# Kernel tuning notes

Measured on AMD Instinct MI355X. Metric: run time of the kernel, lower is better.

## Reference

```python
import jax, jax.numpy as jnp
import numpy as np

DIM = 2048
BATCH = 16384
EPS = 1e-12


def setup_inputs() -> dict:
    key = jax.random.key(0)
    ks = jax.random.split(key, 12)
    d = DIM
    inp = {
        "h_final": jax.random.normal(ks[0], (BATCH, d), dtype=jnp.float32),
        "v_claim": jax.random.normal(ks[1], (BATCH, d), dtype=jnp.float32),
        "v_doc": jax.random.normal(ks[2], (BATCH, d), dtype=jnp.float32),
        # feature_extractor: Linear(d+3, d) -> ReLU -> Linear(d, d//2) -> ReLU
        "W1": jax.random.normal(ks[3], (d + 3, d), dtype=jnp.float32) / np.sqrt(d + 3),
        "b1": jnp.zeros((d,), dtype=jnp.float32),
        "W2": jax.random.normal(ks[4], (d, d // 2), dtype=jnp.float32) / np.sqrt(d),
        "b2": jnp.zeros((d // 2,), dtype=jnp.float32),
        # retrieval head: Linear(d//2, 1) -> Sigmoid
        "Wr": jax.random.normal(ks[5], (d // 2, 1), dtype=jnp.float32) / np.sqrt(d // 2),
        "br": jnp.zeros((1,), dtype=jnp.float32),
    }
    return inp


def reference(h_final, v_claim, v_doc, W1, b1, W2, b2, Wr, br):
    # L2-normalize claim/doc vectors (F.normalize with eps clamp)
    cn = v_claim / jnp.maximum(jnp.linalg.norm(v_claim, axis=-1, keepdims=True), EPS)
    dn = v_doc / jnp.maximum(jnp.linalg.norm(v_doc, axis=-1, keepdims=True), EPS)
    # alignment = cosine similarity (vectors already unit norm) -> [B, 1]
    align = jnp.sum(cn * dn, axis=-1, keepdims=True)
    # divergence = 1 - alignment; tension = divergence^2
    div = 1.0 - align
    tens = div * div
    features = jnp.concatenate([h_final, align, div, tens], axis=-1)  # [B, d+3]
    h = jax.nn.relu(features @ W1 + b1)
    shared = jax.nn.relu(h @ W2 + b2)  # [B, d//2]
    out = jax.nn.sigmoid(shared @ Wr + br)  # [B, 1] (task='retrieval')
    return out
```

## Files before the change

### kernel.cpp

```cpp
#include <hip/hip_runtime.h>
#include <hip/hip_bf16.h>
#include <stdint.h>

#define BATCH 16384
#define DIM   2048
#define DIM2  1024

typedef __attribute__((ext_vector_type(8))) short short8;
typedef __attribute__((ext_vector_type(4))) float f32x4;

__device__ __forceinline__ ushort f2bf(float f) {
  uint32_t u = __float_as_uint(f);
  u += 0x7fffu + ((u >> 16) & 1u);
  return (ushort)(u >> 16);
}
__device__ __forceinline__ float bf2f(ushort h) {
  return __uint_as_float(((uint32_t)h) << 16);
}

__device__ __forceinline__ void gload_lds16(const void* g, void* l) {
  __builtin_amdgcn_global_load_lds(
      (__attribute__((address_space(1))) void*)g,
      (__attribute__((address_space(3))) void*)l,
      16, 0, 0);
}

__device__ __forceinline__ f32x4 MFMA(short8 a, short8 b, f32x4 c) {
  return __builtin_amdgcn_mfma_f32_16x16x32_bf16(a, b, c, 0, 0, 0);
}

__global__ void __launch_bounds__(256) cos_kernel(const float* __restrict__ vc,
                                                  const float* __restrict__ vd,
                                                  float* __restrict__ feats) {
  const int w = threadIdx.x >> 6, l = threadIdx.x & 63;
  const int row = blockIdx.x * 4 + w;
  const float4* c = (const float4*)(vc + (size_t)row * DIM);
  const float4* d = (const float4*)(vd + (size_t)row * DIM);
  float4 ca[8], da[8];
#pragma unroll
  for (int j = 0; j < 8; ++j) ca[j] = c[j * 64 + l];
#pragma unroll
  for (int j = 0; j < 8; ++j) da[j] = d[j * 64 + l];
  float dot = 0.f, c2 = 0.f, d2 = 0.f;
#pragma unroll
  for (int j = 0; j < 8; ++j) {
    float4 a = ca[j], b = da[j];
    dot += a.x * b.x + a.y * b.y + a.z * b.z + a.w * b.w;
    c2  += a.x * a.x + a.y * a.y + a.z * a.z + a.w * a.w;
    d2  += b.x * b.x + b.y * b.y + b.z * b.z + b.w * b.w;
  }
#pragma unroll
  for (int off = 32; off >= 1; off >>= 1) {
    dot += __shfl_xor(dot, off, 64);
    c2  += __shfl_xor(c2, off, 64);
    d2  += __shfl_xor(d2, off, 64);
  }
  if (l == 0) {
    float nc = fmaxf(sqrtf(c2), 1e-12f);
    float nd = fmaxf(sqrtf(d2), 1e-12f);
    float align = dot / (nc * nd);
    float dv = 1.f - align;
    feats[row] = align;
    feats[BATCH + row] = dv;
    feats[2 * BATCH + row] = dv * dv;
  }
}

__global__ void __launch_bounds__(256) cvt_kernel(const float* __restrict__ in,
                                                  ushort* __restrict__ out) {
  const int i0 = blockIdx.x * 256 + threadIdx.x;
  const int S = 8192 * 256;
  const float4* p = (const float4*)in;
  uint2* o = (uint2*)out;
  float4 f[4];
#pragma unroll
  for (int j = 0; j < 4; ++j) f[j] = p[i0 + j * S];
#pragma unroll
  for (int j = 0; j < 4; ++j) {
    uint2 u;
    u.x = (uint32_t)f2bf(f[j].x) | ((uint32_t)f2bf(f[j].y) << 16);
    u.y = (uint32_t)f2bf(f[j].z) | ((uint32_t)f2bf(f[j].w) << 16);
    o[i0 + j * S] = u;
  }
}

__global__ void __launch_bounds__(256) transW(const float* __restrict__ W,
                                              ushort* __restrict__ WT,
                                              int K, int N) {
  __shared__ float tile[32][33];
  int t = threadIdx.x;
  int tx = t & 31, ty = t >> 5;
  int c0 = blockIdx.x * 32, r0 = blockIdx.y * 32;
#pragma unroll
  for (int p = 0; p < 4; ++p)
    tile[ty + p * 8][tx] = W[(size_t)(r0 + ty + p * 8) * N + c0 + tx];
  __syncthreads();
#pragma unroll
  for (int p = 0; p < 4; ++p) {
    int rr = ty + p * 8;
    WT[(size_t)(c0 + rr) * K + r0 + tx] = f2bf(tile[tx][rr]);
  }
}

template <int MODE, int N>
__global__ void __launch_bounds__(512, 1) gemm256(const ushort* __restrict__ A,
                                                  const ushort* __restrict__ BT,
                                                  ushort* __restrict__ C,
                                                  const float* __restrict__ feats,
                                                  const float* __restrict__ wex,
                                                  const float* __restrict__ bias) {
  constexpr int K = 2048;
  constexpr int NT = K / 64;
  __shared__ __align__(16) char lds[131072];
  const int tid = threadIdx.x;
  const int l = tid & 63, w = tid >> 6;
  const int wr = w >> 2, wc = w & 3;
  const int l4 = l & 15, lhi = l >> 4;

  constexpr int GX = N / 256;
  const int bid = blockIdx.x;
  const int xcd = bid & 7;
  const int s = bid >> 3;
  const int tx = s % GX;
  const int ty = xcd * 8 + s / GX;
  const size_t rowBase = (size_t)ty * 256;
  const int colBase = tx * 256;

  const int swz = (l4 & 7) << 4;
  const int aoffBase = l4 * 128 + ((wr * 64 + lhi * 16) ^ swz);
  const int boffBase = ((wc & 1) * 64 + l4) * 128 + (((wc >> 1) * 64 + lhi * 16) ^ swz);

  const char* pAs[2];
  const char* pBs[2];
#pragma unroll
  for (int c = 0; c < 2; ++c) {
    int o = c * 8192 + tid * 16;
    int r = o >> 7, b0 = o & 127;
    int bsw = b0 ^ ((r & 7) << 4);
    int hb = bsw >> 6, cb = bsw & 63;
    pAs[c] = (const char*)A + (rowBase + hb * 128 + r) * (2 * K) + cb;
    pBs[c] = (const char*)BT + ((size_t)colBase + hb * 128 + r) * (2 * K) + cb;
  }
  const int ldso0 = w * 1024;
  const int ldso1 = 8192 + w * 1024;

#define STAGE(srcT, destPar, M, kh)                                          \
  do {                                                                       \
    char* dst_ = lds + (destPar) * 65536 + (kh) * 32768 + (M) * 16384;       \
    const char* s0_ = ((M) ? pBs[0] : pAs[0]) + (srcT) * 128 + (kh) * 64;    \
    const char* s1_ = ((M) ? pBs[1] : pAs[1]) + (srcT) * 128 + (kh) * 64;    \
    gload_lds16(s0_, dst_ + ldso0);                                          \
    gload_lds16(s1_, dst_ + ldso1);                                          \
    asm volatile("" ::: "memory");                                           \
  } while (0)

#define LOADA(q, d, kh)                                                      \
  do {                                                                       \
    const char* sb_ = lds + (d) * 65536 + (kh) * 32768;                      \
    aq[0] = *(const short8*)(sb_ + ((q) * 4 + 0) * 2048 + aoffBase);         \
    aq[1] = *(const short8*)(sb_ + ((q) * 4 + 1) * 2048 + aoffBase);         \
    aq[2] = *(const short8*)(sb_ + ((q) * 4 + 2) * 2048 + aoffBase);         \
    aq[3] = *(const short8*)(sb_ + ((q) * 4 + 3) * 2048 + aoffBase);         \
  } while (0)

#define LOADB(d, kh)                                                         \
  do {                                                                       \
    const char* sb_ = lds + (d) * 65536 + (kh) * 32768 + 16384;              \
    bq[0] = *(const short8*)(sb_ + 0 * 2048 + boffBase);                     \
    bq[1] = *(const short8*)(sb_ + 1 * 2048 + boffBase);                     \
    bq[2] = *(const short8*)(sb_ + 2 * 2048 + boffBase);                     \
    bq[3] = *(const short8*)(sb_ + 3 * 2048 + boffBase);                     \
  } while (0)

#define MF(q)                                                                \
  do {                                                                       \
    _Pragma("unroll") for (int j_ = 0; j_ < 4; ++j_)                         \
        _Pragma("unroll") for (int n_ = 0; n_ < 4; ++n_)                     \
            acc[(q) * 4 + j_][n_] = MFMA(aq[j_], bq[n_], acc[(q) * 4 + j_][n_]); \
  } while (0)

#define BAR()     __builtin_amdgcn_s_barrier()
#define MEMF()    asm volatile("" ::: "memory")
#define VM8()     asm volatile("s_waitcnt vmcnt(8)" ::: "memory")
#define PRIO(x)   __builtin_amdgcn_s_setprio(x)

  f32x4 acc[8][4];
#pragma unroll
  for (int i = 0; i < 8; ++i)
#pragma unroll
    for (int j = 0; j < 4; ++j) acc[i][j] = (f32x4){0.f, 0.f, 0.f, 0.f};

  STAGE(0, 0, 0, 0);
  STAGE(0, 0, 1, 0);
  STAGE(0, 0, 0, 1);
  STAGE(0, 0, 1, 1);
  STAGE(1, 1, 0, 0);
  STAGE(1, 1, 1, 0);
  VM8();
  BAR();
  MEMF();

  for (int I = 0; I < NT / 2; ++I) {
    const int o = 2 * I + 1;
    const int e2 = (2 * I + 2 < NT) ? 2 * I + 2 : 0;
    const int o2 = (2 * I + 3 < NT) ? 2 * I + 3 : 0;
    short8 aq[4], bq[4];
    LOADB(0, 0);
    LOADA(0, 0, 0);
    STAGE(o, 1, 0, 1);
    PRIO(1); MF(0); PRIO(0);
    MEMF(); BAR(); MEMF();
    LOADA(1, 0, 0);
    STAGE(o, 1, 1, 1);
    PRIO(1); MF(1); PRIO(0);
    VM8();
    MEMF(); BAR(); MEMF();
    LOADB(0, 1);
    LOADA(0, 0, 1);
    STAGE(e2, 0, 0, 0);
    PRIO(1); MF(0); PRIO(0);
    MEMF(); BAR(); MEMF();
    LOADA(1, 0, 1);
    STAGE(e2, 0, 1, 0);
    PRIO(1); MF(1); PRIO(0);
    VM8();
    MEMF(); BAR(); MEMF();
    LOADB(1, 0);
    LOADA(0, 1, 0);
    STAGE(e2, 0, 0, 1);
    PRIO(1); MF(0); PRIO(0);
    MEMF(); BAR(); MEMF();
    LOADA(1, 1, 0);
    STAGE(e2, 0, 1, 1);
    PRIO(1); MF(1); PRIO(0);
    VM8();
    MEMF(); BAR(); MEMF();
    LOADB(1, 1);
    LOADA(0, 1, 1);
    STAGE(o2, 1, 0, 0);
    PRIO(1); MF(0); PRIO(0);
    MEMF(); BAR(); MEMF();
    LOADA(1, 1, 1);
    STAGE(o2, 1, 1, 0);
    PRIO(1); MF(1); PRIO(0);
    VM8();
    MEMF(); BAR(); MEMF();
  }
  asm volatile("s_waitcnt vmcnt(0)" ::: "memory");

  int ccv[4];
  float bb[4], wa[4], wb2[4], wc3[4];
#pragma unroll
  for (int n = 0; n < 4; ++n) {
    int cc = colBase + wc * 64 + n * 16 + l4;
    ccv[n] = cc;
    bb[n] = bias[cc];
    if (MODE == 1) {
      wa[n] = wex[cc]; wb2[n] = wex[2048 + cc]; wc3[n] = wex[4096 + cc];
    } else {
      wa[n] = 0.f; wb2[n] = 0.f; wc3[n] = 0.f;
    }
  }
  const int lhi4 = lhi * 4;
#pragma unroll
  for (int m = 0; m < 8; ++m) {
#pragma unroll
    for (int r = 0; r < 4; ++r) {
      size_t rr = rowBase + wr * 128 + m * 16 + lhi4 + r;
      float f1 = 0.f, f2 = 0.f, f3 = 0.f;
      if (MODE == 1) {
        f1 = feats[rr]; f2 = feats[BATCH + rr]; f3 = feats[2 * BATCH + rr];
      }
#pragma unroll
      for (int n = 0; n < 4; ++n) {
        float v = acc[m][n][r] + bb[n];
        if (MODE == 1) v += f1 * wa[n] + f2 * wb2[n] + f3 * wc3[n];
        v = fmaxf(v, 0.f);
        C[rr * N + ccv[n]] = f2bf(v);
      }
    }
  }
#undef STAGE
#undef LOADA
#undef LOADB
#undef MF
#undef BAR
#undef MEMF
#undef VM8
#undef PRIO
}

__global__ void __launch_bounds__(256) head_kernel(const ushort* __restrict__ S,
                                                   const float* __restrict__ Wr,
                                                   const float* __restrict__ br,
                                                   float* __restrict__ out) {
  int row = blockIdx.x * 4 + (threadIdx.x >> 6);
  int l = threadIdx.x & 63;
  const ushort* s = S + (size_t)row * DIM2 + l * 16;
  const float4* wp = (const float4*)(Wr + l * 16);
  uint4 u0 = *(const uint4*)s;
  uint4 u1 = *(const uint4*)(s + 8);
  float4 w0 = wp[0], w1 = wp[1], w2 = wp[2], w3 = wp[3];
  float sum = 0.f;
  sum += bf2f((ushort)(u0.x & 0xffff)) * w0.x + bf2f((ushort)(u0.x >> 16)) * w0.y;
  sum += bf2f((ushort)(u0.y & 0xffff)) * w0.z + bf2f((ushort)(u0.y >> 16)) * w0.w;
  sum += bf2f((ushort)(u0.z & 0xffff)) * w1.x + bf2f((ushort)(u0.z >> 16)) * w1.y;
  sum += bf2f((ushort)(u0.w & 0xffff)) * w1.z + bf2f((ushort)(u0.w >> 16)) * w1.w;
  sum += bf2f((ushort)(u1.x & 0xffff)) * w2.x + bf2f((ushort)(u1.x >> 16)) * w2.y;
  sum += bf2f((ushort)(u1.y & 0xffff)) * w2.z + bf2f((ushort)(u1.y >> 16)) * w2.w;
  sum += bf2f((ushort)(u1.z & 0xffff)) * w3.x + bf2f((ushort)(u1.z >> 16)) * w3.y;
  sum += bf2f((ushort)(u1.w & 0xffff)) * w3.z + bf2f((ushort)(u1.w >> 16)) * w3.w;
#pragma unroll
  for (int off = 32; off >= 1; off >>= 1) sum += __shfl_down(sum, off, 64);
  if (l == 0) out[row] = 1.f / (1.f + expf(-(sum + br[0])));
}

extern "C" void kernel_launch(void* const* d_in, const int* in_sizes, int n_in,
                              void* d_out, int out_size, void* d_ws, size_t ws_size,
                              hipStream_t stream) {
  const float* h_final = (const float*)d_in[0];
  const float* v_claim = (const float*)d_in[1];
  const float* v_doc   = (const float*)d_in[2];
  const float* W1      = (const float*)d_in[3];
  const float* b1      = (const float*)d_in[4];
  const float* W2      = (const float*)d_in[5];
  const float* b2      = (const float*)d_in[6];
  const float* Wr      = (const float*)d_in[7];
  const float* br      = (const float*)d_in[8];
  float* out = (float*)d_out;

  char* ws = (char*)d_ws;
  ushort* Abf   = (ushort*)ws;
  ushort* Hbf   = (ushort*)(ws + 67108864);
  ushort* W1T   = (ushort*)(ws + 134217728);
  ushort* W2T   = (ushort*)(ws + 142606336);
  float*  feats = (float*)(ws + 146800640);
  ushort* Sbf   = Abf;

  cos_kernel<<<BATCH / 4, 256, 0, stream>>>(v_claim, v_doc, feats);
  cvt_kernel<<<8192, 256, 0, stream>>>(h_final, Abf);
  transW<<<dim3(DIM / 32, DIM / 32), 256, 0, stream>>>(W1, W1T, DIM, DIM);
  transW<<<dim3(DIM2 / 32, DIM / 32), 256, 0, stream>>>(W2, W2T, DIM, DIM2);

  gemm256<1, DIM><<<(DIM / 256) * (BATCH / 256), 512, 0, stream>>>(
      Abf, W1T, Hbf, feats, W1 + (size_t)2048 * 2048, b1);
  gemm256<2, DIM2><<<(DIM2 / 256) * (BATCH / 256), 512, 0, stream>>>(
      Hbf, W2T, Sbf, nullptr, nullptr, b2);

  head_kernel<<<BATCH / 4, 256, 0, stream>>>(Sbf, Wr, br, out);
}
```

Baseline: 286.6 us.

## Switch GEMM inner product from 16x16x32 to 32x32x16 bf16 MFMA tiles

Replaces the 16x16x32 bf16 MFMA with the 32x32x16 variant. The LDS fragment addressing, swizzle offsets, accumulator layout and epilogue row/column mapping are all remapped to match. Larger MFMA tiles halve the number of LDS fragment reads per FLOP and issue fewer, larger matrix instructions, which is meant to raise throughput. The per-wave 128x64 tile stays the same, and the new addressing could change LDS bank conflicts.

```diff
diff --git a/kernel.cpp b/kernel.cpp
--- a/kernel.cpp
+++ b/kernel.cpp
@@ -8,6 +8,7 @@
 
 typedef __attribute__((ext_vector_type(8))) short short8;
 typedef __attribute__((ext_vector_type(4))) float f32x4;
+typedef __attribute__((ext_vector_type(16))) float f32x16;
 
 __device__ __forceinline__ ushort f2bf(float f) {
   uint32_t u = __float_as_uint(f);
@@ -25,8 +26,8 @@
       16, 0, 0);
 }
 
-__device__ __forceinline__ f32x4 MFMA(short8 a, short8 b, f32x4 c) {
-  return __builtin_amdgcn_mfma_f32_16x16x32_bf16(a, b, c, 0, 0, 0);
+__device__ __forceinline__ f32x16 MFMA32(short8 a, short8 b, f32x16 c) {
+  return __builtin_amdgcn_mfma_f32_32x32x16_bf16(a, b, c, 0, 0, 0);
 }
 
 __global__ void __launch_bounds__(256) cos_kernel(const float* __restrict__ vc,
@@ -115,7 +116,7 @@
   const int tid = threadIdx.x;
   const int l = tid & 63, w = tid >> 6;
   const int wr = w >> 2, wc = w & 3;
-  const int l4 = l & 15, lhi = l >> 4;
+  const int lr = l & 31, l5 = l >> 5, x7 = l & 7;
 
   constexpr int GX = N / 256;
   const int bid = blockIdx.x;
@@ -126,9 +127,10 @@
   const size_t rowBase = (size_t)ty * 256;
   const int colBase = tx * 256;
 
-  const int swz = (l4 & 7) << 4;
-  const int aoffBase = l4 * 128 + ((wr * 64 + lhi * 16) ^ swz);
-  const int boffBase = ((wc & 1) * 64 + l4) * 128 + (((wc >> 1) * 64 + lhi * 16) ^ swz);
+  const int aoff0 = lr * 128 + 16 * (((wr << 2) + 0 + l5) ^ x7);
+  const int aoff1 = lr * 128 + 16 * (((wr << 2) + 2 + l5) ^ x7);
+  const int boff0 = ((wc & 1) * 64 + lr) * 128 + 16 * ((((wc >> 1) << 2) + 0 + l5) ^ x7);
+  const int boff1 = ((wc & 1) * 64 + lr) * 128 + 16 * ((((wc >> 1) << 2) + 2 + l5) ^ x7);
 
   const char* pAs[2];
   const char* pBs[2];
@@ -156,27 +158,29 @@
 
 #define LOADA(q, d, kh)                                                      \
   do {                                                                       \
-    const char* sb_ = lds + (d) * 65536 + (kh) * 32768;                      \
-    aq[0] = *(const short8*)(sb_ + ((q) * 4 + 0) * 2048 + aoffBase);         \
-    aq[1] = *(const short8*)(sb_ + ((q) * 4 + 1) * 2048 + aoffBase);         \
-    aq[2] = *(const short8*)(sb_ + ((q) * 4 + 2) * 2048 + aoffBase);         \
-    aq[3] = *(const short8*)(sb_ + ((q) * 4 + 3) * 2048 + aoffBase);         \
+    const char* sb_ = lds + (d) * 65536 + (kh) * 32768 + (q) * 8192;         \
+    aq[0][0] = *(const short8*)(sb_ + 0    + aoff0);                         \
+    aq[0][1] = *(const short8*)(sb_ + 0    + aoff1);                         \
+    aq[1][0] = *(const short8*)(sb_ + 4096 + aoff0);                         \
+    aq[1][1] = *(const short8*)(sb_ + 4096 + aoff1);                         \
   } while (0)
 
 #define LOADB(d, kh)                                                         \
   do {                                                                       \
     const char* sb_ = lds + (d) * 65536 + (kh) * 32768 + 16384;              \
-    bq[0] = *(const short8*)(sb_ + 0 * 2048 + boffBase);                     \
-    bq[1] = *(const short8*)(sb_ + 1 * 2048 + boffBase);                     \
-    bq[2] = *(const short8*)(sb_ + 2 * 2048 + boffBase);                     \
-    bq[3] = *(const short8*)(sb_ + 3 * 2048 + boffBase);                     \
+    bq[0][0] = *(const short8*)(sb_ + 0    + boff0);                         \
+    bq[0][1] = *(const short8*)(sb_ + 0    + boff1);                         \
+    bq[1][0] = *(const short8*)(sb_ + 4096 + boff0);                         \
+    bq[1][1] = *(const short8*)(sb_ + 4096 + boff1);                         \
   } while (0)
 
 #define MF(q)                                                                \
   do {                                                                       \
-    _Pragma("unroll") for (int j_ = 0; j_ < 4; ++j_)                         \
-        _Pragma("unroll") for (int n_ = 0; n_ < 4; ++n_)                     \
-            acc[(q) * 4 + j_][n_] = MFMA(aq[j_], bq[n_], acc[(q) * 4 + j_][n_]); \
+    _Pragma("unroll") for (int s_ = 0; s_ < 2; ++s_)                         \
+      _Pragma("unroll") for (int r_ = 0; r_ < 2; ++r_)                       \
+        _Pragma("unroll") for (int c_ = 0; c_ < 2; ++c_)                     \
+          acc[(q) * 2 + r_][c_] =                                            \
+              MFMA32(aq[r_][s_], bq[c_][s_], acc[(q) * 2 + r_][c_]);         \
   } while (0)
 
 #define BAR()     __builtin_amdgcn_s_barrier()
@@ -184,11 +188,13 @@
 #define VM8()     asm volatile("s_waitcnt vmcnt(8)" ::: "memory")
 #define PRIO(x)   __builtin_amdgcn_s_setprio(x)
 
-  f32x4 acc[8][4];
-#pragma unroll
-  for (int i = 0; i < 8; ++i)
-#pragma unroll
-    for (int j = 0; j < 4; ++j) acc[i][j] = (f32x4){0.f, 0.f, 0.f, 0.f};
+  f32x16 acc[4][2];
+#pragma unroll
+  for (int i = 0; i < 4; ++i)
+#pragma unroll
+    for (int j = 0; j < 2; ++j)
+#pragma unroll
+      for (int e = 0; e < 16; ++e) acc[i][j][e] = 0.f;
 
   STAGE(0, 0, 0, 0);
   STAGE(0, 0, 1, 0);
@@ -204,7 +210,7 @@
     const int o = 2 * I + 1;
     const int e2 = (2 * I + 2 < NT) ? 2 * I + 2 : 0;
     const int o2 = (2 * I + 3 < NT) ? 2 * I + 3 : 0;
-    short8 aq[4], bq[4];
+    short8 aq[2][2], bq[2][2];
     LOADB(0, 0);
     LOADA(0, 0, 0);
     STAGE(o, 1, 0, 1);
@@ -248,35 +254,34 @@
   }
   asm volatile("s_waitcnt vmcnt(0)" ::: "memory");
 
-  int ccv[4];
-  float bb[4], wa[4], wb2[4], wc3[4];
-#pragma unroll
-  for (int n = 0; n < 4; ++n) {
-    int cc = colBase + wc * 64 + n * 16 + l4;
-    ccv[n] = cc;
-    bb[n] = bias[cc];
+  int ccv[2];
+  float bb[2], wa[2], wb2[2], wc3[2];
+#pragma unroll
+  for (int ct = 0; ct < 2; ++ct) {
+    int cc = colBase + wc * 64 + ct * 32 + lr;
+    ccv[ct] = cc;
+    bb[ct] = bias[cc];
     if (MODE == 1) {
-      wa[n] = wex[cc]; wb2[n] = wex[2048 + cc]; wc3[n] = wex[4096 + cc];
+      wa[ct] = wex[cc]; wb2[ct] = wex[2048 + cc]; wc3[ct] = wex[4096 + cc];
     } else {
-      wa[n] = 0.f; wb2[n] = 0.f; wc3[n] = 0.f;
+      wa[ct] = 0.f; wb2[ct] = 0.f; wc3[ct] = 0.f;
     }
   }
-  const int lhi4 = lhi * 4;
-#pragma unroll
-  for (int m = 0; m < 8; ++m) {
-#pragma unroll
-    for (int r = 0; r < 4; ++r) {
-      size_t rr = rowBase + wr * 128 + m * 16 + lhi4 + r;
+#pragma unroll
+  for (int rt = 0; rt < 4; ++rt) {
+#pragma unroll
+    for (int reg = 0; reg < 16; ++reg) {
+      size_t rr = rowBase + wr * 128 + rt * 32 + (reg & 3) + 8 * (reg >> 2) + 4 * l5;
       float f1 = 0.f, f2 = 0.f, f3 = 0.f;
       if (MODE == 1) {
         f1 = feats[rr]; f2 = feats[BATCH + rr]; f3 = feats[2 * BATCH + rr];
       }
 #pragma unroll
-      for (int n = 0; n < 4; ++n) {
-        float v = acc[m][n][r] + bb[n];
-        if (MODE == 1) v += f1 * wa[n] + f2 * wb2[n] + f3 * wc3[n];
+      for (int ct = 0; ct < 2; ++ct) {
+        float v = acc[rt][ct][reg] + bb[ct];
+        if (MODE == 1) v += f1 * wa[ct] + f2 * wb2[ct] + f3 * wc3[ct];
         v = fmaxf(v, 0.f);
-        C[rr * N + ccv[n]] = f2bf(v);
+        C[rr * N + ccv[ct]] = f2bf(v);
       }
     }
   }
```

Result: slower. 303.4 us (+5.9%).

## Use 4-wave blocks with 128x128 per-wave tiles and simpler GEMM pipeline

Applied to the files above, without the earlier changes.

Switches the GEMM kernel from 8 waves of 128x64 warp tiles to 4 waves each computing a 128x128 sub-tile, doubling accumulators per wave and raising MFMA-to-LDS-read ratio. Staging now issues four 16B global-to-LDS loads per thread per stage, and the main loop is restructured into four phases with one barrier each, fetching one k-tile ahead. This reduces LDS traffic and barriers per MFMA but leaves only one wave per SIMD, reducing latency hiding and greatly increasing register pressure (256 accumulator registers).

```diff
diff --git a/kernel.cpp b/kernel.cpp
--- a/kernel.cpp
+++ b/kernel.cpp
@@ -103,7 +103,7 @@
 }
 
 template <int MODE, int N>
-__global__ void __launch_bounds__(512, 1) gemm256(const ushort* __restrict__ A,
+__global__ void __launch_bounds__(256, 1) gemm256(const ushort* __restrict__ A,
                                                   const ushort* __restrict__ BT,
                                                   ushort* __restrict__ C,
                                                   const float* __restrict__ feats,
@@ -114,7 +114,7 @@
   __shared__ __align__(16) char lds[131072];
   const int tid = threadIdx.x;
   const int l = tid & 63, w = tid >> 6;
-  const int wr = w >> 2, wc = w & 3;
+  const int wr = w >> 1, wc = w & 1;
   const int l4 = l & 15, lhi = l >> 4;
 
   constexpr int GX = N / 256;
@@ -128,55 +128,54 @@
 
   const int swz = (l4 & 7) << 4;
   const int aoffBase = l4 * 128 + ((wr * 64 + lhi * 16) ^ swz);
-  const int boffBase = ((wc & 1) * 64 + l4) * 128 + (((wc >> 1) * 64 + lhi * 16) ^ swz);
-
-  const char* pAs[2];
-  const char* pBs[2];
-#pragma unroll
-  for (int c = 0; c < 2; ++c) {
-    int o = c * 8192 + tid * 16;
+  const int boffBase = l4 * 128 + ((wc * 64 + lhi * 16) ^ swz);
+
+  const char* pAs[4];
+  const char* pBs[4];
+#pragma unroll
+  for (int c = 0; c < 4; ++c) {
+    int o = c * 4096 + tid * 16;
     int r = o >> 7, b0 = o & 127;
     int bsw = b0 ^ ((r & 7) << 4);
     int hb = bsw >> 6, cb = bsw & 63;
     pAs[c] = (const char*)A + (rowBase + hb * 128 + r) * (2 * K) + cb;
     pBs[c] = (const char*)BT + ((size_t)colBase + hb * 128 + r) * (2 * K) + cb;
   }
-  const int ldso0 = w * 1024;
-  const int ldso1 = 8192 + w * 1024;
+  const int wB = w * 1024;
 
 #define STAGE(srcT, destPar, M, kh)                                          \
   do {                                                                       \
-    char* dst_ = lds + (destPar) * 65536 + (kh) * 32768 + (M) * 16384;       \
+    char* dst_ = lds + (destPar) * 65536 + (kh) * 32768 + (M) * 16384 + wB;  \
     const char* s0_ = ((M) ? pBs[0] : pAs[0]) + (srcT) * 128 + (kh) * 64;    \
     const char* s1_ = ((M) ? pBs[1] : pAs[1]) + (srcT) * 128 + (kh) * 64;    \
-    gload_lds16(s0_, dst_ + ldso0);                                          \
-    gload_lds16(s1_, dst_ + ldso1);                                          \
+    const char* s2_ = ((M) ? pBs[2] : pAs[2]) + (srcT) * 128 + (kh) * 64;    \
+    const char* s3_ = ((M) ? pBs[3] : pAs[3]) + (srcT) * 128 + (kh) * 64;    \
+    gload_lds16(s0_, dst_);                                                  \
+    gload_lds16(s1_, dst_ + 4096);                                           \
+    gload_lds16(s2_, dst_ + 8192);                                           \
+    gload_lds16(s3_, dst_ + 12288);                                          \
     asm volatile("" ::: "memory");                                           \
   } while (0)
 
-#define LOADA(q, d, kh)                                                      \
+#define LOADA(d, kh)                                                         \
   do {                                                                       \
     const char* sb_ = lds + (d) * 65536 + (kh) * 32768;                      \
-    aq[0] = *(const short8*)(sb_ + ((q) * 4 + 0) * 2048 + aoffBase);         \
-    aq[1] = *(const short8*)(sb_ + ((q) * 4 + 1) * 2048 + aoffBase);         \
-    aq[2] = *(const short8*)(sb_ + ((q) * 4 + 2) * 2048 + aoffBase);         \
-    aq[3] = *(const short8*)(sb_ + ((q) * 4 + 3) * 2048 + aoffBase);         \
+    _Pragma("unroll") for (int i_ = 0; i_ < 8; ++i_)                         \
+        aq[i_] = *(const short8*)(sb_ + i_ * 2048 + aoffBase);               \
   } while (0)
 
 #define LOADB(d, kh)                                                         \
   do {                                                                       \
     const char* sb_ = lds + (d) * 65536 + (kh) * 32768 + 16384;              \
-    bq[0] = *(const short8*)(sb_ + 0 * 2048 + boffBase);                     \
-    bq[1] = *(const short8*)(sb_ + 1 * 2048 + boffBase);                     \
-    bq[2] = *(const short8*)(sb_ + 2 * 2048 + boffBase);                     \
-    bq[3] = *(const short8*)(sb_ + 3 * 2048 + boffBase);                     \
+    _Pragma("unroll") for (int n_ = 0; n_ < 8; ++n_)                         \
+        bq[n_] = *(const short8*)(sb_ + n_ * 2048 + boffBase);               \
   } while (0)
 
-#define MF(q)                                                                \
+#define MFR()                                                                \
   do {                                                                       \
-    _Pragma("unroll") for (int j_ = 0; j_ < 4; ++j_)                         \
-        _Pragma("unroll") for (int n_ = 0; n_ < 4; ++n_)                     \
-            acc[(q) * 4 + j_][n_] = MFMA(aq[j_], bq[n_], acc[(q) * 4 + j_][n_]); \
+    _Pragma("unroll") for (int j_ = 0; j_ < 8; ++j_)                         \
+        _Pragma("unroll") for (int n_ = 0; n_ < 8; ++n_)                     \
+            acc[j_][n_] = MFMA(aq[j_], bq[n_], acc[j_][n_]);                 \
   } while (0)
 
 #define BAR()     __builtin_amdgcn_s_barrier()
@@ -184,18 +183,16 @@
 #define VM8()     asm volatile("s_waitcnt vmcnt(8)" ::: "memory")
 #define PRIO(x)   __builtin_amdgcn_s_setprio(x)
 
-  f32x4 acc[8][4];
+  f32x4 acc[8][8];
 #pragma unroll
   for (int i = 0; i < 8; ++i)
 #pragma unroll
-    for (int j = 0; j < 4; ++j) acc[i][j] = (f32x4){0.f, 0.f, 0.f, 0.f};
+    for (int j = 0; j < 8; ++j) acc[i][j] = (f32x4){0.f, 0.f, 0.f, 0.f};
 
   STAGE(0, 0, 0, 0);
   STAGE(0, 0, 1, 0);
   STAGE(0, 0, 0, 1);
   STAGE(0, 0, 1, 1);
-  STAGE(1, 1, 0, 0);
-  STAGE(1, 1, 1, 0);
   VM8();
   BAR();
   MEMF();
@@ -203,56 +200,31 @@
   for (int I = 0; I < NT / 2; ++I) {
     const int o = 2 * I + 1;
     const int e2 = (2 * I + 2 < NT) ? 2 * I + 2 : 0;
-    const int o2 = (2 * I + 3 < NT) ? 2 * I + 3 : 0;
-    short8 aq[4], bq[4];
-    LOADB(0, 0);
-    LOADA(0, 0, 0);
-    STAGE(o, 1, 0, 1);
-    PRIO(1); MF(0); PRIO(0);
-    MEMF(); BAR(); MEMF();
-    LOADA(1, 0, 0);
-    STAGE(o, 1, 1, 1);
-    PRIO(1); MF(1); PRIO(0);
-    VM8();
-    MEMF(); BAR(); MEMF();
-    LOADB(0, 1);
-    LOADA(0, 0, 1);
-    STAGE(e2, 0, 0, 0);
-    PRIO(1); MF(0); PRIO(0);
-    MEMF(); BAR(); MEMF();
-    LOADA(1, 0, 1);
-    STAGE(e2, 0, 1, 0);
-    PRIO(1); MF(1); PRIO(0);
-    VM8();
-    MEMF(); BAR(); MEMF();
-    LOADB(1, 0);
-    LOADA(0, 1, 0);
-    STAGE(e2, 0, 0, 1);
-    PRIO(1); MF(0); PRIO(0);
-    MEMF(); BAR(); MEMF();
-    LOADA(1, 1, 0);
-    STAGE(e2, 0, 1, 1);
-    PRIO(1); MF(1); PRIO(0);
-    VM8();
-    MEMF(); BAR(); MEMF();
-    LOADB(1, 1);
-    LOADA(0, 1, 1);
-    STAGE(o2, 1, 0, 0);
-    PRIO(1); MF(0); PRIO(0);
-    MEMF(); BAR(); MEMF();
-    LOADA(1, 1, 1);
-    STAGE(o2, 1, 1, 0);
-    PRIO(1); MF(1); PRIO(0);
-    VM8();
-    MEMF(); BAR(); MEMF();
+    short8 aq[8], bq[8];
+    LOADB(0, 0); LOADA(0, 0);
+    STAGE(o, 1, 0, 0); STAGE(o, 1, 1, 0);
+    PRIO(1); MFR(); PRIO(0);
+    VM8(); MEMF(); BAR(); MEMF();
+    LOADB(0, 1); LOADA(0, 1);
+    STAGE(o, 1, 0, 1); STAGE(o, 1, 1, 1);
+    PRIO(1); MFR(); PRIO(0);
+    VM8(); MEMF(); BAR(); MEMF();
+    LOADB(1, 0); LOADA(1, 0);
+    STAGE(e2, 0, 0, 0); STAGE(e2, 0, 1, 0);
+    PRIO(1); MFR(); PRIO(0);
+    VM8(); MEMF(); BAR(); MEMF();
+    LOADB(1, 1); LOADA(1, 1);
+    STAGE(e2, 0, 0, 1); STAGE(e2, 0, 1, 1);
+    PRIO(1); MFR(); PRIO(0);
+    VM8(); MEMF(); BAR(); MEMF();
   }
   asm volatile("s_waitcnt vmcnt(0)" ::: "memory");
 
-  int ccv[4];
-  float bb[4], wa[4], wb2[4], wc3[4];
-#pragma unroll
-  for (int n = 0; n < 4; ++n) {
-    int cc = colBase + wc * 64 + n * 16 + l4;
+  int ccv[8];
+  float bb[8], wa[8], wb2[8], wc3[8];
+#pragma unroll
+  for (int n = 0; n < 8; ++n) {
+    int cc = colBase + wc * 128 + n * 16 + l4;
     ccv[n] = cc;
     bb[n] = bias[cc];
     if (MODE == 1) {
@@ -272,7 +244,7 @@
         f1 = feats[rr]; f2 = feats[BATCH + rr]; f3 = feats[2 * BATCH + rr];
       }
 #pragma unroll
-      for (int n = 0; n < 4; ++n) {
+      for (int n = 0; n < 8; ++n) {
         float v = acc[m][n][r] + bb[n];
         if (MODE == 1) v += f1 * wa[n] + f2 * wb2[n] + f3 * wc3[n];
         v = fmaxf(v, 0.f);
@@ -283,7 +255,7 @@
 #undef STAGE
 #undef LOADA
 #undef LOADB
-#undef MF
+#undef MFR
 #undef BAR
 #undef MEMF
 #undef VM8
@@ -342,9 +314,9 @@
   transW<<<dim3(DIM / 32, DIM / 32), 256, 0, stream>>>(W1, W1T, DIM, DIM);
   transW<<<dim3(DIM2 / 32, DIM / 32), 256, 0, stream>>>(W2, W2T, DIM, DIM2);
 
-  gemm256<1, DIM><<<(DIM / 256) * (BATCH / 256), 512, 0, stream>>>(
+  gemm256<1, DIM><<<(DIM / 256) * (BATCH / 256), 256, 0, stream>>>(
       Abf, W1T, Hbf, feats, W1 + (size_t)2048 * 2048, b1);
-  gemm256<2, DIM2><<<(DIM2 / 256) * (BATCH / 256), 512, 0, stream>>>(
+  gemm256<2, DIM2><<<(DIM2 / 256) * (BATCH / 256), 256, 0, stream>>>(
       Hbf, W2T, Sbf, nullptr, nullptr, b2);
 
   head_kernel<<<BATCH / 4, 256, 0, stream>>>(Sbf, Wr, br, out);
```

New measurement: 381.8 us. 1.33x slower.

## Fuse retrieval head dot-product into second GEMM epilogue via per-row partial sums

Applied to the files above, without the earlier changes.

The second GEMM epilogue no longer writes the bf16 shared activations. Instead it applies bias and ReLU, multiplies by the head weights, and reduces across lanes into 16 partial sums per row. A tiny kernel then sums the partials and applies the sigmoid. This removes a 32 MB activation write and its read-back by the old head kernel, at the cost of extra shuffles in the epilogue and a small partial buffer placed in the W1T workspace region, which is dead after the first GEMM.

```diff
diff --git a/kernel.cpp b/kernel.cpp
--- a/kernel.cpp
+++ b/kernel.cpp
@@ -108,7 +108,9 @@
                                                   ushort* __restrict__ C,
                                                   const float* __restrict__ feats,
                                                   const float* __restrict__ wex,
-                                                  const float* __restrict__ bias) {
+                                                  const float* __restrict__ bias,
+                                                  const float* __restrict__ Wr,
+                                                  float* __restrict__ partial) {
   constexpr int K = 2048;
   constexpr int NT = K / 64;
   __shared__ __align__(16) char lds[131072];
@@ -248,35 +250,53 @@
   }
   asm volatile("s_waitcnt vmcnt(0)" ::: "memory");
 
-  int ccv[4];
-  float bb[4], wa[4], wb2[4], wc3[4];
-#pragma unroll
-  for (int n = 0; n < 4; ++n) {
-    int cc = colBase + wc * 64 + n * 16 + l4;
-    ccv[n] = cc;
-    bb[n] = bias[cc];
-    if (MODE == 1) {
+  const int lhi4 = lhi * 4;
+  if (MODE == 1) {
+    int ccv[4];
+    float bb[4], wa[4], wb2[4], wc3[4];
+#pragma unroll
+    for (int n = 0; n < 4; ++n) {
+      int cc = colBase + wc * 64 + n * 16 + l4;
+      ccv[n] = cc;
+      bb[n] = bias[cc];
       wa[n] = wex[cc]; wb2[n] = wex[2048 + cc]; wc3[n] = wex[4096 + cc];
-    } else {
-      wa[n] = 0.f; wb2[n] = 0.f; wc3[n] = 0.f;
     }
-  }
-  const int lhi4 = lhi * 4;
-#pragma unroll
-  for (int m = 0; m < 8; ++m) {
-#pragma unroll
-    for (int r = 0; r < 4; ++r) {
-      size_t rr = rowBase + wr * 128 + m * 16 + lhi4 + r;
-      float f1 = 0.f, f2 = 0.f, f3 = 0.f;
-      if (MODE == 1) {
-        f1 = feats[rr]; f2 = feats[BATCH + rr]; f3 = feats[2 * BATCH + rr];
+#pragma unroll
+    for (int m = 0; m < 8; ++m) {
+#pragma unroll
+      for (int r = 0; r < 4; ++r) {
+        size_t rr = rowBase + wr * 128 + m * 16 + lhi4 + r;
+        float f1 = feats[rr], f2 = feats[BATCH + rr], f3 = feats[2 * BATCH + rr];
+#pragma unroll
+        for (int n = 0; n < 4; ++n) {
+          float v = acc[m][n][r] + bb[n] + f1 * wa[n] + f2 * wb2[n] + f3 * wc3[n];
+          v = fmaxf(v, 0.f);
+          C[rr * N + ccv[n]] = f2bf(v);
+        }
       }
-#pragma unroll
-      for (int n = 0; n < 4; ++n) {
-        float v = acc[m][n][r] + bb[n];
-        if (MODE == 1) v += f1 * wa[n] + f2 * wb2[n] + f3 * wc3[n];
-        v = fmaxf(v, 0.f);
-        C[rr * N + ccv[n]] = f2bf(v);
+    }
+  } else {
+    float bb[4], wrv[4];
+#pragma unroll
+    for (int n = 0; n < 4; ++n) {
+      int cc = colBase + wc * 64 + n * 16 + l4;
+      bb[n] = bias[cc];
+      wrv[n] = Wr[cc];
+    }
+#pragma unroll
+    for (int m = 0; m < 8; ++m) {
+#pragma unroll
+      for (int r = 0; r < 4; ++r) {
+        size_t rr = rowBase + wr * 128 + m * 16 + lhi4 + r;
+        float p = 0.f;
+#pragma unroll
+        for (int n = 0; n < 4; ++n)
+          p += fmaxf(acc[m][n][r] + bb[n], 0.f) * wrv[n];
+        p += __shfl_xor(p, 1, 64);
+        p += __shfl_xor(p, 2, 64);
+        p += __shfl_xor(p, 4, 64);
+        p += __shfl_xor(p, 8, 64);
+        if (l4 == 0) partial[rr * 16 + tx * 4 + wc] = p;
       }
     }
   }
@@ -290,29 +310,15 @@
 #undef PRIO
 }
 
-__global__ void __launch_bounds__(256) head_kernel(const ushort* __restrict__ S,
-                                                   const float* __restrict__ Wr,
-                                                   const float* __restrict__ br,
-                                                   float* __restrict__ out) {
-  int row = blockIdx.x * 4 + (threadIdx.x >> 6);
-  int l = threadIdx.x & 63;
-  const ushort* s = S + (size_t)row * DIM2 + l * 16;
-  const float4* wp = (const float4*)(Wr + l * 16);
-  uint4 u0 = *(const uint4*)s;
-  uint4 u1 = *(const uint4*)(s + 8);
-  float4 w0 = wp[0], w1 = wp[1], w2 = wp[2], w3 = wp[3];
-  float sum = 0.f;
-  sum += bf2f((ushort)(u0.x & 0xffff)) * w0.x + bf2f((ushort)(u0.x >> 16)) * w0.y;
-  sum += bf2f((ushort)(u0.y & 0xffff)) * w0.z + bf2f((ushort)(u0.y >> 16)) * w0.w;
-  sum += bf2f((ushort)(u0.z & 0xffff)) * w1.x + bf2f((ushort)(u0.z >> 16)) * w1.y;
-  sum += bf2f((ushort)(u0.w & 0xffff)) * w1.z + bf2f((ushort)(u0.w >> 16)) * w1.w;
-  sum += bf2f((ushort)(u1.x & 0xffff)) * w2.x + bf2f((ushort)(u1.x >> 16)) * w2.y;
-  sum += bf2f((ushort)(u1.y & 0xffff)) * w2.z + bf2f((ushort)(u1.y >> 16)) * w2.w;
-  sum += bf2f((ushort)(u1.z & 0xffff)) * w3.x + bf2f((ushort)(u1.z >> 16)) * w3.y;
-  sum += bf2f((ushort)(u1.w & 0xffff)) * w3.z + bf2f((ushort)(u1.w >> 16)) * w3.w;
-#pragma unroll
-  for (int off = 32; off >= 1; off >>= 1) sum += __shfl_down(sum, off, 64);
-  if (l == 0) out[row] = 1.f / (1.f + expf(-(sum + br[0])));
+__global__ void __launch_bounds__(256) head2_kernel(const float* __restrict__ partial,
+                                                    const float* __restrict__ br,
+                                                    float* __restrict__ out) {
+  int row = blockIdx.x * 256 + threadIdx.x;
+  const float4* p = (const float4*)(partial + (size_t)row * 16);
+  float4 a = p[0], b = p[1], c = p[2], d = p[3];
+  float s = a.x + a.y + a.z + a.w + b.x + b.y + b.z + b.w +
+            c.x + c.y + c.z + c.w + d.x + d.y + d.z + d.w + br[0];
+  out[row] = 1.f / (1.f + expf(-s));
 }
 
 extern "C" void kernel_launch(void* const* d_in, const int* in_sizes, int n_in,
@@ -335,7 +341,7 @@
   ushort* W1T   = (ushort*)(ws + 134217728);
   ushort* W2T   = (ushort*)(ws + 142606336);
   float*  feats = (float*)(ws + 146800640);
-  ushort* Sbf   = Abf;
+  float*  partial = (float*)(ws + 134217728);
 
   cos_kernel<<<BATCH / 4, 256, 0, stream>>>(v_claim, v_doc, feats);
   cvt_kernel<<<8192, 256, 0, stream>>>(h_final, Abf);
@@ -343,9 +349,9 @@
   transW<<<dim3(DIM2 / 32, DIM / 32), 256, 0, stream>>>(W2, W2T, DIM, DIM2);
 
   gemm256<1, DIM><<<(DIM / 256) * (BATCH / 256), 512, 0, stream>>>(
-      Abf, W1T, Hbf, feats, W1 + (size_t)2048 * 2048, b1);
+      Abf, W1T, Hbf, feats, W1 + (size_t)2048 * 2048, b1, nullptr, nullptr);
   gemm256<2, DIM2><<<(DIM2 / 256) * (BATCH / 256), 512, 0, stream>>>(
-      Hbf, W2T, Sbf, nullptr, nullptr, b2);
-
-  head_kernel<<<BATCH / 4, 256, 0, stream>>>(Sbf, Wr, br, out);
-}
+      Hbf, W2T, nullptr, nullptr, nullptr, b2, Wr, partial);
+
+  head2_kernel<<<BATCH / 256, 256, 0, stream>>>(partial, br, out);
+}
```

Result: faster. 275.8 us (-3.7%).
